# Kernel optimization log

Hardware: AMD Instinct MI355X
Metric: run time of the kernel (lower is better)

## Reference

```python
import jax, jax.numpy as jnp
import numpy as np

# Model config (matches init_kwargs)
DIM = 2048
INTER = 1408          # moe_inter_dim
E = 16                # n_routed_experts
TOPK = 4              # n_activated_experts
G = 4                 # n_expert_groups
TOPK_G = 2            # n_limited_groups
N_SHARED = 2
SHARED_INTER = N_SHARED * INTER  # 2816
ROUTE_SCALE = 1.0


def setup_inputs() -> dict:
    key = jax.random.key(0)
    ks = jax.random.split(key, 8)
    s = 0.02
    x = jax.random.normal(ks[0], (1, 2048, DIM), dtype=jnp.float32)
    Wg = jax.random.normal(ks[1], (E, DIM), dtype=jnp.float32) * s      # gate weight
    W1 = jax.random.normal(ks[2], (E, INTER, DIM), dtype=jnp.float32) * s  # expert gate proj
    W3 = jax.random.normal(ks[3], (E, INTER, DIM), dtype=jnp.float32) * s  # expert up proj
    W2 = jax.random.normal(ks[4], (E, DIM, INTER), dtype=jnp.float32) * s  # expert down proj
    Ws1 = jax.random.normal(ks[5], (SHARED_INTER, DIM), dtype=jnp.float32) * s
    Ws3 = jax.random.normal(ks[6], (SHARED_INTER, DIM), dtype=jnp.float32) * s
    Ws2 = jax.random.normal(ks[7], (DIM, SHARED_INTER), dtype=jnp.float32) * s
    return {"x": x, "Wg": Wg, "W1": W1, "W3": W3, "W2": W2,
            "Ws1": Ws1, "Ws3": Ws3, "Ws2": Ws2}


def _moe_forward(x, Wg, W1, W3, W2, Ws1, Ws3, Ws2):
    B, S, D = x.shape
    xt = x.reshape(-1, D)              # [T, D]
    T = xt.shape[0]

    # ---- Gate: group-limited top-k routing (bias is None since dim != 7168) ----
    scores = jax.nn.softmax(xt @ Wg.T, axis=-1)          # [T, E]
    sg = scores.reshape(T, G, E // G)                    # [T, G, E/G]
    group_scores = sg.max(axis=-1)                       # amax per group
    gidx = jax.lax.top_k(group_scores, TOPK_G)[1]        # [T, TOPK_G]
    gmask = jax.nn.one_hot(gidx, G, dtype=jnp.float32).sum(axis=1) > 0  # [T, G] kept groups
    masked = jnp.where(gmask[:, :, None], sg, -jnp.inf).reshape(T, E)
    topi = jax.lax.top_k(masked, TOPK)[1]                # [T, TOPK] expert indices
    weights = jnp.take_along_axis(scores, topi, axis=1) * ROUTE_SCALE  # original_scores gather

    # ---- Routed experts: dense per-expert SwiGLU FFN, zero-weight combine ----
    # combine[t, e] = sum over k of weights[t, k] * (topi[t, k] == e)
    combine = jnp.zeros((T, E), xt.dtype).at[jnp.arange(T)[:, None], topi].add(weights)
    h = jax.nn.silu(jnp.einsum('td,eid->eti', xt, W1)) * jnp.einsum('td,eid->eti', xt, W3)
    expert_out = jnp.einsum('eti,edi->etd', h, W2)       # [E, T, D]
    y = jnp.einsum('etd,te->td', expert_out, combine)    # [T, D]

    # ---- Shared expert (applied to all tokens) ----
    z = (jax.nn.silu(xt @ Ws1.T) * (xt @ Ws3.T)) @ Ws2.T

    return (y + z).reshape(B, S, D)


def reference(x, Wg, W1, W3, W2, Ws1, Ws3, Ws2):
    return _moe_forward(x, Wg, W1, W3, W2, Ws1, Ws3, Ws2)
```

## Files before the change

kernel.cpp:

```cpp
#include <hip/hip_runtime.h>
#include <stdint.h>

#define D_MODEL  2048
#define N_INTER  1408
#define SH_INTER 2816
#define T_TOK    2048
#define NSLOT    (T_TOK * 4)
#define MIB(x)   ((size_t)(x) << 20)

typedef __attribute__((ext_vector_type(8))) short bf16x8;
typedef __attribute__((ext_vector_type(4))) float f32x4;

__device__ __forceinline__ unsigned short f2bf(float f){
  unsigned int b = __builtin_bit_cast(unsigned int, f);
  b = (b + 0x7FFFu + ((b >> 16) & 1u)) >> 16;
  return (unsigned short)b;
}
__device__ __forceinline__ float bf2f(unsigned short h){
  unsigned int b = ((unsigned int)h) << 16;
  return __builtin_bit_cast(float, b);
}

#define GLOAD16(gp, lp) __builtin_amdgcn_global_load_lds( \
    (const __attribute__((address_space(1))) unsigned int*)(gp), \
    (__attribute__((address_space(3))) unsigned int*)(lp), 16, 0, 0)

__global__ void cvt_bf16_kernel(const float* __restrict__ x,
                                unsigned short* __restrict__ o, int n4){
  const int stride = gridDim.x * blockDim.x;
  for (int i = blockIdx.x * blockDim.x + threadIdx.x; i < n4; i += stride){
    const float4 v = ((const float4*)x)[i];
    ushort4 u; u.x = f2bf(v.x); u.y = f2bf(v.y); u.z = f2bf(v.z); u.w = f2bf(v.w);
    ((ushort4*)o)[i] = u;
  }
}

__global__ void cvt4_kernel(const float* __restrict__ x,  const float* __restrict__ Ws1,
                            const float* __restrict__ Ws3, const float* __restrict__ Ws2,
                            unsigned short* __restrict__ xbf, unsigned short* __restrict__ S1,
                            unsigned short* __restrict__ S3,  unsigned short* __restrict__ S2){
  const int N0 = T_TOK * D_MODEL / 4;
  const int NW = SH_INTER * D_MODEL / 4;
  const int total = N0 + 3 * NW;
  const int stride = gridDim.x * blockDim.x;
  for (int i = blockIdx.x * blockDim.x + threadIdx.x; i < total; i += stride){
    const float4* s; ushort4* d; int j;
    if (i < N0)            { s = (const float4*)x;   d = (ushort4*)xbf; j = i; }
    else if (i < N0 + NW)  { s = (const float4*)Ws1; d = (ushort4*)S1;  j = i - N0; }
    else if (i < N0 + 2*NW){ s = (const float4*)Ws3; d = (ushort4*)S3;  j = i - N0 - NW; }
    else                   { s = (const float4*)Ws2; d = (ushort4*)S2;  j = i - N0 - 2*NW; }
    const float4 v = s[j];
    ushort4 u; u.x = f2bf(v.x); u.y = f2bf(v.y); u.z = f2bf(v.z); u.w = f2bf(v.w);
    d[j] = u;
  }
}

__global__ void gate_kernel(const float* __restrict__ x, const float* __restrict__ Wg,
                            int* __restrict__ cnt, int* __restrict__ list,
                            float* __restrict__ wslot){
  const int t = blockIdx.x;
  const int l = threadIdx.x;
  const int e = l & 15, q = l >> 4;
  const float* xr = x + (size_t)t * D_MODEL + q * 512;
  const float* wr = Wg + (size_t)e * D_MODEL + q * 512;
  float p = 0.f;
  #pragma unroll 4
  for (int i = 0; i < 512; i += 4){
    float4 xv = *(const float4*)(xr + i);
    float4 wv = *(const float4*)(wr + i);
    p += xv.x*wv.x + xv.y*wv.y + xv.z*wv.z + xv.w*wv.w;
  }
  p += __shfl_xor(p, 16);
  p += __shfl_xor(p, 32);
  float mx = p;
  for (int d = 1; d < 16; d <<= 1) mx = fmaxf(mx, __shfl_xor(mx, d));
  float ex = __expf(p - mx);
  float sum = ex;
  for (int d = 1; d < 16; d <<= 1) sum += __shfl_xor(sum, d);
  const float sc = ex / sum;
  float gm = fmaxf(sc, __shfl_xor(sc, 1));
  gm = fmaxf(gm, __shfl_xor(gm, 2));
  const float g0 = __shfl(gm, 0), g1 = __shfl(gm, 4),
              g2 = __shfl(gm, 8), g3 = __shfl(gm, 12);
  const int grp = e >> 2;
  const float gs[4] = {g0, g1, g2, g3};
  int grank = 0;
  #pragma unroll
  for (int j = 0; j < 4; ++j)
    if (gs[j] > gm || (gs[j] == gm && j < grp)) grank++;
  const float msc = (grank < 2) ? sc : -INFINITY;
  int erank = 0;
  #pragma unroll
  for (int j = 0; j < 16; ++j){
    const float oj = __shfl(msc, j);
    if (oj > msc || (oj == msc && j < e)) erank++;
  }
  if (q == 0 && erank < 4 && msc > -INFINITY){
    const int pos = atomicAdd(&cnt[e], 1);
    const int slot = (t << 2) | erank;
    list[e * T_TOK + pos] = slot;
    wslot[slot] = sc;
  }
}

template<int MODE, int KS>
__global__ __launch_bounds__(512, 2)
void gemm8_kernel(const unsigned short* __restrict__ A,
                  const unsigned short* __restrict__ BG,
                  const unsigned short* __restrict__ BU,
                  void* __restrict__ OutP,
                  const int* __restrict__ list,
                  const int* __restrict__ cnt,
                  int K, int N, int NI, int MT, int NT)
{
  constexpr bool GATHER = (MODE == 2 || MODE == 3);
  constexpr bool GU     = (MODE == 0 || MODE == 2);
  __shared__ unsigned short As[3 * 8192];
  __shared__ unsigned short Bs[3 * 8192];

  const int per = gridDim.x >> 3;
  const int gsw = (blockIdx.x & 7) * per + (blockIdx.x >> 3);
  const int mt = gsw % MT;
  const int rest = gsw / MT;
  const int nt = rest % NT;
  const int rest2 = rest / NT;
  const int ks = (KS > 1) ? (rest2 % KS) : 0;
  const int e  = GATHER ? rest2 : 0;
  const int cntE = GATHER ? cnt[e] : (MT * 256);
  if (mt * 256 >= cntE) return;

  const int tid = threadIdx.x, wid = tid >> 6, lane = tid & 63;
  const int sx   = ((lane & 3) ^ ((lane >> 3) & 3)) << 3;
  const int kOff = (KS > 1) ? ks * (K / KS) : 0;

  const int rt0 = 32 * wid + (lane >> 2), rt1 = rt0 + 16;
  int ar0, ar1;
  if (GATHER){
    const int lim = cntE - 1;
    int p0 = mt * 256 + rt0; p0 = p0 < lim ? p0 : lim;
    int p1 = mt * 256 + rt1; p1 = p1 < lim ? p1 : lim;
    const int e0 = list[e * T_TOK + p0], e1 = list[e * T_TOK + p1];
    ar0 = (MODE == 2) ? (e0 >> 2) : e0;
    ar1 = (MODE == 2) ? (e1 >> 2) : e1;
  } else { ar0 = mt * 256 + rt0; ar1 = mt * 256 + rt1; }
  const unsigned short* pa0 = A + (size_t)ar0 * K + kOff + sx;
  const unsigned short* pa1 = A + (size_t)ar1 * K + kOff + sx;

  const unsigned short* pb0;
  const unsigned short* pb1;
  if (GU){
    const size_t eo = GATHER ? (size_t)e * NI * K : 0;
    const int g0 = nt * 256 + rt0, g1 = nt * 256 + rt1;
    pb0 = (g0 < NI ? BG + eo + (size_t)g0 * K : BU + eo + (size_t)(g0 - NI) * K) + sx;
    pb1 = (g1 < NI ? BG + eo + (size_t)g1 * K : BU + eo + (size_t)(g1 - NI) * K) + sx;
  } else {
    const unsigned short* base = BG + (GATHER ? (size_t)e * N * K : 0) + kOff;
    pb0 = base + (size_t)(nt * 256 + rt0) * K + sx;
    pb1 = base + (size_t)(nt * 256 + rt1) * K + sx;
  }

  const int w0 = (32 * wid) * 32, w1 = w0 + 512;
  const int bufStr = 8192;

  const int wm = wid >> 2, wn = wid & 3, lr = lane & 15, lq = lane >> 4;
  const int fx = (lq ^ ((lr >> 1) & 3)) << 3;
  int aoff[8], boff[4];
  #pragma unroll
  for (int m = 0; m < 8; ++m) aoff[m] = (wm * 128 + m * 16 + lr) * 32 + fx;
  #pragma unroll
  for (int n = 0; n < 4; ++n) boff[n] = (wn * 64 + n * 16 + lr) * 32 + fx;

  f32x4 acc[8][4];
  const f32x4 zero = {0.f, 0.f, 0.f, 0.f};
  #pragma unroll
  for (int m = 0; m < 8; ++m)
    #pragma unroll
    for (int n = 0; n < 4; ++n) acc[m][n] = zero;

  const int KT = (K / (KS > 1 ? KS : 1)) >> 5;
  #pragma unroll
  for (int t = 0; t < 3; ++t){
    GLOAD16(pa0, As + t * bufStr + w0);
    GLOAD16(pa1, As + t * bufStr + w1);
    GLOAD16(pb0, Bs + t * bufStr + w0);
    GLOAD16(pb1, Bs + t * bufStr + w1);
    pa0 += 32; pa1 += 32; pb0 += 32; pb1 += 32;
  }
  int c = 0;

  for (int kt = 0; kt < KT; ++kt){
    if (kt < KT - 2)       asm volatile("s_waitcnt vmcnt(8)" ::: "memory");
    else if (kt == KT - 2) asm volatile("s_waitcnt vmcnt(4)" ::: "memory");
    else                   asm volatile("s_waitcnt vmcnt(0)" ::: "memory");
    __builtin_amdgcn_s_barrier();

    const unsigned short* aC = As + c * bufStr;
    const unsigned short* bC = Bs + c * bufStr;
    bf16x8 af[8], bf[4];
    #pragma unroll
    for (int m = 0; m < 8; ++m) af[m] = *(const bf16x8*)(aC + aoff[m]);
    #pragma unroll
    for (int n = 0; n < 4; ++n) bf[n] = *(const bf16x8*)(bC + boff[n]);

    asm volatile("s_waitcnt lgkmcnt(0)" ::: "memory");
    __builtin_amdgcn_sched_barrier(0);
    __builtin_amdgcn_s_barrier();

    if (kt + 3 < KT){
      GLOAD16(pa0, As + c * bufStr + w0);
      GLOAD16(pa1, As + c * bufStr + w1);
      GLOAD16(pb0, Bs + c * bufStr + w0);
      GLOAD16(pb1, Bs + c * bufStr + w1);
      pa0 += 32; pa1 += 32; pb0 += 32; pb1 += 32;
    }

    __builtin_amdgcn_s_setprio(1);
    #pragma unroll
    for (int n = 0; n < 4; ++n)
      #pragma unroll
      for (int m = 0; m < 8; ++m)
        acc[m][n] = __builtin_amdgcn_mfma_f32_16x16x32_bf16(af[m], bf[n], acc[m][n], 0, 0, 0);
    __builtin_amdgcn_s_setprio(0);

    c = (c == 2) ? 0 : c + 1;
  }

  const int colBase = nt * 256 + wn * 64;
  #pragma unroll
  for (int m = 0; m < 8; ++m){
    #pragma unroll
    for (int r = 0; r < 4; ++r){
      const int grow = mt * 256 + wm * 128 + m * 16 + lq * 4 + r;
      if (MODE == 1){
        float* op = (float*)OutP + (size_t)ks * MT * 256 * N + (size_t)grow * N + colBase;
        #pragma unroll
        for (int n = 0; n < 4; ++n) op[n * 16 + lr] = acc[m][n][r];
      } else if (MODE == 0){
        unsigned short* op = (unsigned short*)OutP + (size_t)grow * N + colBase;
        #pragma unroll
        for (int n = 0; n < 4; ++n) op[n * 16 + lr] = f2bf(acc[m][n][r]);
      } else {
        if (grow >= cntE) continue;
        const int orow = list[e * T_TOK + grow];
        unsigned short* op = (unsigned short*)OutP + (size_t)orow * N + colBase;
        #pragma unroll
        for (int n = 0; n < 4; ++n) op[n * 16 + lr] = f2bf(acc[m][n][r]);
      }
    }
  }
}

__global__ void swiglu_split_kernel(const unsigned short* __restrict__ GU,
                                    unsigned short* __restrict__ H,
                                    int n8, int NI8){
  const int stride = gridDim.x * blockDim.x;
  for (int i = blockIdx.x * blockDim.x + threadIdx.x; i < n8; i += stride){
    const int r = i / NI8, ccol = i - r * NI8;
    const bf16x8 g = ((const bf16x8*)GU)[(size_t)r * 2 * NI8 + ccol];
    const bf16x8 u = ((const bf16x8*)GU)[(size_t)r * 2 * NI8 + NI8 + ccol];
    bf16x8 h;
    #pragma unroll
    for (int j = 0; j < 8; ++j){
      const float gv = bf2f((unsigned short)g[j]);
      const float uv = bf2f((unsigned short)u[j]);
      h[j] = (short)f2bf(gv / (1.f + __expf(-gv)) * uv);
    }
    ((bf16x8*)H)[i] = h;
  }
}

__global__ void combine_kernel(const unsigned short* __restrict__ H2,
                               const float* __restrict__ P,
                               const float* __restrict__ wslot,
                               float* __restrict__ out){
  const int t = blockIdx.x;
  const int ccol = threadIdx.x * 8;
  float w[4];
  #pragma unroll
  for (int k = 0; k < 4; ++k) w[k] = wslot[t * 4 + k];
  float a[8];
  #pragma unroll
  for (int j = 0; j < 8; ++j) a[j] = 0.f;
  #pragma unroll
  for (int p = 0; p < 4; ++p){
    const float* pp = P + (size_t)(p * T_TOK + t) * D_MODEL + ccol;
    #pragma unroll
    for (int j = 0; j < 8; ++j) a[j] += pp[j];
  }
  #pragma unroll
  for (int k = 0; k < 4; ++k){
    const bf16x8 hv = *(const bf16x8*)(H2 + (size_t)(t * 4 + k) * D_MODEL + ccol);
    #pragma unroll
    for (int j = 0; j < 8; ++j) a[j] += w[k] * bf2f((unsigned short)hv[j]);
  }
  float* o = out + (size_t)t * D_MODEL + ccol;
  #pragma unroll
  for (int j = 0; j < 8; ++j) o[j] = a[j];
}

extern "C" void kernel_launch(void* const* d_in, const int* in_sizes, int n_in,
                              void* d_out, int out_size, void* d_ws, size_t ws_size,
                              hipStream_t stream)
{
  const float* x   = (const float*)d_in[0];
  const float* Wg  = (const float*)d_in[1];
  const float* W1  = (const float*)d_in[2];
  const float* W3  = (const float*)d_in[3];
  const float* W2  = (const float*)d_in[4];
  const float* Ws1 = (const float*)d_in[5];
  const float* Ws3 = (const float*)d_in[6];
  const float* Ws2 = (const float*)d_in[7];
  float* out = (float*)d_out;

  char* ws = (char*)d_ws;
  int*   cnt   = (int*)(ws);
  int*   list  = (int*)(ws + 4096);
  float* wslot = (float*)(ws + 4096 + 131072);
  unsigned short* xbf  = (unsigned short*)(ws + MIB(1));
  unsigned short* S1   = (unsigned short*)(ws + MIB(10));
  unsigned short* S3   = (unsigned short*)(ws + MIB(22));
  unsigned short* S2   = (unsigned short*)(ws + MIB(34));
  unsigned short* Hs   = (unsigned short*)(ws + MIB(46));
  unsigned short* GU_s = (unsigned short*)(ws + MIB(58));
  unsigned short* Hr   = (unsigned short*)(ws + MIB(82));
  unsigned short* Hc   = (unsigned short*)(ws + MIB(129));
  unsigned short* H2   = (unsigned short*)(ws + MIB(153));
  float*          P    = (float*)        (ws + MIB(187));
  unsigned short* W1b  = (unsigned short*)(ws + MIB(255));
  unsigned short* W3b  = (unsigned short*)(ws + MIB(348));
  unsigned short* W2b  = (unsigned short*)(ws + MIB(441));

  const int NW_R = 16 * N_INTER * D_MODEL / 4;

  hipMemsetAsync(cnt, 0, 4096, stream);
  cvt4_kernel<<<2048, 256, 0, stream>>>(x, Ws1, Ws3, Ws2, xbf, S1, S3, S2);
  gate_kernel<<<T_TOK, 64, 0, stream>>>(x, Wg, cnt, list, wslot);

  gemm8_kernel<0, 1><<<176, 512, 0, stream>>>(xbf, S1, S3, GU_s, nullptr, nullptr,
                                              D_MODEL, 2 * SH_INTER, SH_INTER, 8, 22);
  cvt_bf16_kernel<<<4096, 256, 0, stream>>>(W1, W1b, NW_R);
  cvt_bf16_kernel<<<4096, 256, 0, stream>>>(W3, W3b, NW_R);
  swiglu_split_kernel<<<2048, 256, 0, stream>>>(GU_s, Hs, T_TOK * SH_INTER / 8, SH_INTER / 8);

  gemm8_kernel<1, 4><<<256, 512, 0, stream>>>(Hs, S2, nullptr, P, nullptr, nullptr,
                                              SH_INTER, D_MODEL, 0, 8, 8);

  gemm8_kernel<2, 1><<<1408, 512, 0, stream>>>(xbf, W1b, W3b, Hr, list, cnt,
                                               D_MODEL, 2 * N_INTER, N_INTER, 8, 11);
  cvt_bf16_kernel<<<4096, 256, 0, stream>>>(W2, W2b, NW_R);
  swiglu_split_kernel<<<2048, 256, 0, stream>>>(Hr, Hc, NSLOT * N_INTER / 8, N_INTER / 8);

  gemm8_kernel<3, 1><<<1024, 512, 0, stream>>>(Hc, W2b, nullptr, H2, list, cnt,
                                               N_INTER, D_MODEL, 0, 8, 8);

  combine_kernel<<<T_TOK, 256, 0, stream>>>(H2, P, wslot, out);
}
```

Baseline: 734.6 us.

## Restructure GEMM into double-buffered 64-wide K pipeline with concatenated gate/up weights

Measured after the change: 624.7 us. 15.0% less time.

```diff
diff --git a/kernel.cpp b/kernel.cpp
--- a/kernel.cpp
+++ b/kernel.cpp
@@ -32,6 +32,19 @@
     const float4 v = ((const float4*)x)[i];
     ushort4 u; u.x = f2bf(v.x); u.y = f2bf(v.y); u.z = f2bf(v.z); u.w = f2bf(v.w);
     ((ushort4*)o)[i] = u;
+  }
+}
+
+__global__ void cvt_routed_kernel(const float* __restrict__ src,
+                                  unsigned short* __restrict__ dst,
+                                  int n4, int nik4, int off4){
+  const int stride = gridDim.x * blockDim.x;
+  for (int i = blockIdx.x * blockDim.x + threadIdx.x; i < n4; i += stride){
+    const int e = i / nik4;
+    const int r = i - e * nik4;
+    const float4 v = ((const float4*)src)[i];
+    ushort4 u; u.x = f2bf(v.x); u.y = f2bf(v.y); u.z = f2bf(v.z); u.w = f2bf(v.w);
+    ((ushort4*)dst)[(size_t)e * 2 * nik4 + off4 + r] = u;
   }
 }
 
@@ -104,160 +117,189 @@
 }
 
 template<int MODE, int KS>
-__global__ __launch_bounds__(512, 2)
-void gemm8_kernel(const unsigned short* __restrict__ A,
-                  const unsigned short* __restrict__ BG,
-                  const unsigned short* __restrict__ BU,
-                  void* __restrict__ OutP,
-                  const int* __restrict__ list,
-                  const int* __restrict__ cnt,
-                  int K, int N, int NI, int MT, int NT)
+__global__ __launch_bounds__(512, 1)
+void gemm8p_kernel(const unsigned short* __restrict__ A,
+                   const unsigned short* __restrict__ B,
+                   void* __restrict__ OutP,
+                   const int* __restrict__ list,
+                   const int* __restrict__ cnt,
+                   int K, int N, int Astride, size_t eBstride,
+                   int MT, int NT)
 {
   constexpr bool GATHER = (MODE == 2 || MODE == 3);
-  constexpr bool GU     = (MODE == 0 || MODE == 2);
-  __shared__ unsigned short As[3 * 8192];
-  __shared__ unsigned short Bs[3 * 8192];
+  __shared__ unsigned short LDS[65536];
 
   const int per = gridDim.x >> 3;
   const int gsw = (blockIdx.x & 7) * per + (blockIdx.x >> 3);
   const int mt = gsw % MT;
-  const int rest = gsw / MT;
-  const int nt = rest % NT;
-  const int rest2 = rest / NT;
-  const int ks = (KS > 1) ? (rest2 % KS) : 0;
-  const int e  = GATHER ? rest2 : 0;
+  int rest = gsw / MT;
+  const int nt = rest % NT; rest /= NT;
+  const int ks = (KS > 1) ? (rest % KS) : 0;
+  const int e  = GATHER ? ((KS > 1) ? rest / KS : rest) : 0;
   const int cntE = GATHER ? cnt[e] : (MT * 256);
   if (mt * 256 >= cntE) return;
 
   const int tid = threadIdx.x, wid = tid >> 6, lane = tid & 63;
-  const int sx   = ((lane & 3) ^ ((lane >> 3) & 3)) << 3;
   const int kOff = (KS > 1) ? ks * (K / KS) : 0;
-
-  const int rt0 = 32 * wid + (lane >> 2), rt1 = rt0 + 16;
-  int ar0, ar1;
-  if (GATHER){
-    const int lim = cntE - 1;
-    int p0 = mt * 256 + rt0; p0 = p0 < lim ? p0 : lim;
-    int p1 = mt * 256 + rt1; p1 = p1 < lim ? p1 : lim;
-    const int e0 = list[e * T_TOK + p0], e1 = list[e * T_TOK + p1];
-    ar0 = (MODE == 2) ? (e0 >> 2) : e0;
-    ar1 = (MODE == 2) ? (e1 >> 2) : e1;
-  } else { ar0 = mt * 256 + rt0; ar1 = mt * 256 + rt1; }
-  const unsigned short* pa0 = A + (size_t)ar0 * K + kOff + sx;
-  const unsigned short* pa1 = A + (size_t)ar1 * K + kOff + sx;
-
-  const unsigned short* pb0;
-  const unsigned short* pb1;
-  if (GU){
-    const size_t eo = GATHER ? (size_t)e * NI * K : 0;
-    const int g0 = nt * 256 + rt0, g1 = nt * 256 + rt1;
-    pb0 = (g0 < NI ? BG + eo + (size_t)g0 * K : BU + eo + (size_t)(g0 - NI) * K) + sx;
-    pb1 = (g1 < NI ? BG + eo + (size_t)g1 * K : BU + eo + (size_t)(g1 - NI) * K) + sx;
-  } else {
-    const unsigned short* base = BG + (GATHER ? (size_t)e * N * K : 0) + kOff;
-    pb0 = base + (size_t)(nt * 256 + rt0) * K + sx;
-    pb1 = base + (size_t)(nt * 256 + rt1) * K + sx;
-  }
-
-  const int w0 = (32 * wid) * 32, w1 = w0 + 512;
-  const int bufStr = 8192;
+  const int sx = ((lane & 3) ^ ((lane >> 3) & 3)) << 3;
+
+  const unsigned short* pa[2];
+  const unsigned short* pb[2];
+  const unsigned short* Bb = B + (GATHER ? (size_t)e * eBstride : 0);
+  #pragma unroll
+  for (int j = 0; j < 2; ++j){
+    const int rl = (2 * wid + j) * 16 + (lane >> 2);
+    int ga;
+    if (GATHER){
+      int p = mt * 256 + rl;
+      const int lim = cntE - 1;
+      p = p < lim ? p : lim;
+      const int en = list[e * T_TOK + p];
+      ga = (MODE == 2) ? (en >> 2) : en;
+    } else ga = mt * 256 + rl;
+    pa[j] = A + (size_t)ga * Astride + kOff + sx;
+    pb[j] = Bb + (size_t)(nt * 256 + rl) * K + kOff + sx;
+  }
+  const int dW0 = (2 * wid) * 512, dW1 = dW0 + 512;
 
   const int wm = wid >> 2, wn = wid & 3, lr = lane & 15, lq = lane >> 4;
   const int fx = (lq ^ ((lr >> 1) & 3)) << 3;
-  int aoff[8], boff[4];
-  #pragma unroll
-  for (int m = 0; m < 8; ++m) aoff[m] = (wm * 128 + m * 16 + lr) * 32 + fx;
-  #pragma unroll
-  for (int n = 0; n < 4; ++n) boff[n] = (wn * 64 + n * 16 + lr) * 32 + fx;
+  int aoff0[4], aoff1[4], boff[4];
+  #pragma unroll
+  for (int m = 0; m < 4; ++m){
+    aoff0[m] = (wm * 128 + m * 16 + lr) * 32 + fx;
+    aoff1[m] = (wm * 128 + 64 + m * 16 + lr) * 32 + fx;
+  }
+  #pragma unroll
+  for (int n = 0; n < 4; ++n) boff[n] = 16384 + (wn * 64 + n * 16 + lr) * 32 + fx;
 
   f32x4 acc[8][4];
   const f32x4 zero = {0.f, 0.f, 0.f, 0.f};
   #pragma unroll
-  for (int m = 0; m < 8; ++m)
-    #pragma unroll
-    for (int n = 0; n < 4; ++n) acc[m][n] = zero;
-
-  const int KT = (K / (KS > 1 ? KS : 1)) >> 5;
-  #pragma unroll
-  for (int t = 0; t < 3; ++t){
-    GLOAD16(pa0, As + t * bufStr + w0);
-    GLOAD16(pa1, As + t * bufStr + w1);
-    GLOAD16(pb0, Bs + t * bufStr + w0);
-    GLOAD16(pb1, Bs + t * bufStr + w1);
-    pa0 += 32; pa1 += 32; pb0 += 32; pb1 += 32;
-  }
-  int c = 0;
-
-  for (int kt = 0; kt < KT; ++kt){
-    if (kt < KT - 2)       asm volatile("s_waitcnt vmcnt(8)" ::: "memory");
-    else if (kt == KT - 2) asm volatile("s_waitcnt vmcnt(4)" ::: "memory");
-    else                   asm volatile("s_waitcnt vmcnt(0)" ::: "memory");
-    __builtin_amdgcn_s_barrier();
-
-    const unsigned short* aC = As + c * bufStr;
-    const unsigned short* bC = Bs + c * bufStr;
-    bf16x8 af[8], bf[4];
-    #pragma unroll
-    for (int m = 0; m < 8; ++m) af[m] = *(const bf16x8*)(aC + aoff[m]);
-    #pragma unroll
-    for (int n = 0; n < 4; ++n) bf[n] = *(const bf16x8*)(bC + boff[n]);
-
+  for (int M = 0; M < 8; ++M)
+    #pragma unroll
+    for (int n = 0; n < 4; ++n) acc[M][n] = zero;
+
+  const int KT = (K / (KS > 1 ? KS : 1)) >> 6;
+
+  GLOAD16(pa[0],      &LDS[dW0]);
+  GLOAD16(pa[1],      &LDS[dW1]);
+  GLOAD16(pb[0],      &LDS[16384 + dW0]);
+  GLOAD16(pb[1],      &LDS[16384 + dW1]);
+  GLOAD16(pa[0] + 32, &LDS[8192 + dW0]);
+  GLOAD16(pa[1] + 32, &LDS[8192 + dW1]);
+  GLOAD16(pb[0] + 32, &LDS[16384 + 8192 + dW0]);
+  GLOAD16(pb[1] + 32, &LDS[16384 + 8192 + dW1]);
+
+  for (int t = 0; t < KT; ++t){
+    const int bb = (t & 1) << 15;
+    const int db = bb ^ 32768;
+    const bool more = (t + 1) < KT;
+    const size_t ko = (size_t)(t + 1) * 64;
+    bf16x8 af[4], bq[4];
+
+    asm volatile("s_waitcnt vmcnt(4)" ::: "memory");
+    __builtin_amdgcn_s_barrier();
+    #pragma unroll
+    for (int m = 0; m < 4; ++m) af[m] = *(const bf16x8*)(&LDS[bb + aoff0[m]]);
+    #pragma unroll
+    for (int n = 0; n < 4; ++n) bq[n] = *(const bf16x8*)(&LDS[bb + boff[n]]);
+    if (more){ GLOAD16(pa[0] + ko, &LDS[db + dW0]); GLOAD16(pa[1] + ko, &LDS[db + dW1]); }
     asm volatile("s_waitcnt lgkmcnt(0)" ::: "memory");
     __builtin_amdgcn_sched_barrier(0);
-    __builtin_amdgcn_s_barrier();
-
-    if (kt + 3 < KT){
-      GLOAD16(pa0, As + c * bufStr + w0);
-      GLOAD16(pa1, As + c * bufStr + w1);
-      GLOAD16(pb0, Bs + c * bufStr + w0);
-      GLOAD16(pb1, Bs + c * bufStr + w1);
-      pa0 += 32; pa1 += 32; pb0 += 32; pb1 += 32;
-    }
-
     __builtin_amdgcn_s_setprio(1);
     #pragma unroll
     for (int n = 0; n < 4; ++n)
       #pragma unroll
-      for (int m = 0; m < 8; ++m)
-        acc[m][n] = __builtin_amdgcn_mfma_f32_16x16x32_bf16(af[m], bf[n], acc[m][n], 0, 0, 0);
+      for (int m = 0; m < 4; ++m)
+        acc[m][n] = __builtin_amdgcn_mfma_f32_16x16x32_bf16(af[m], bq[n], acc[m][n], 0, 0, 0);
     __builtin_amdgcn_s_setprio(0);
-
-    c = (c == 2) ? 0 : c + 1;
+    __builtin_amdgcn_s_barrier();
+
+    #pragma unroll
+    for (int m = 0; m < 4; ++m) af[m] = *(const bf16x8*)(&LDS[bb + aoff1[m]]);
+    if (more){ GLOAD16(pb[0] + ko, &LDS[db + 16384 + dW0]);
+               GLOAD16(pb[1] + ko, &LDS[db + 16384 + dW1]); }
+    asm volatile("s_waitcnt lgkmcnt(0)" ::: "memory");
+    __builtin_amdgcn_sched_barrier(0);
+    __builtin_amdgcn_s_setprio(1);
+    #pragma unroll
+    for (int n = 0; n < 4; ++n)
+      #pragma unroll
+      for (int m = 0; m < 4; ++m)
+        acc[4 + m][n] = __builtin_amdgcn_mfma_f32_16x16x32_bf16(af[m], bq[n], acc[4 + m][n], 0, 0, 0);
+    __builtin_amdgcn_s_setprio(0);
+    __builtin_amdgcn_s_barrier();
+
+    if (more) asm volatile("s_waitcnt vmcnt(4)" ::: "memory");
+    else      asm volatile("s_waitcnt vmcnt(0)" ::: "memory");
+    __builtin_amdgcn_s_barrier();
+    #pragma unroll
+    for (int m = 0; m < 4; ++m) af[m] = *(const bf16x8*)(&LDS[bb + 8192 + aoff0[m]]);
+    #pragma unroll
+    for (int n = 0; n < 4; ++n) bq[n] = *(const bf16x8*)(&LDS[bb + 8192 + boff[n]]);
+    if (more){ GLOAD16(pa[0] + ko + 32, &LDS[db + 8192 + dW0]);
+               GLOAD16(pa[1] + ko + 32, &LDS[db + 8192 + dW1]); }
+    asm volatile("s_waitcnt lgkmcnt(0)" ::: "memory");
+    __builtin_amdgcn_sched_barrier(0);
+    __builtin_amdgcn_s_setprio(1);
+    #pragma unroll
+    for (int n = 0; n < 4; ++n)
+      #pragma unroll
+      for (int m = 0; m < 4; ++m)
+        acc[m][n] = __builtin_amdgcn_mfma_f32_16x16x32_bf16(af[m], bq[n], acc[m][n], 0, 0, 0);
+    __builtin_amdgcn_s_setprio(0);
+    __builtin_amdgcn_s_barrier();
+
+    #pragma unroll
+    for (int m = 0; m < 4; ++m) af[m] = *(const bf16x8*)(&LDS[bb + 8192 + aoff1[m]]);
+    if (more){ GLOAD16(pb[0] + ko + 32, &LDS[db + 16384 + 8192 + dW0]);
+               GLOAD16(pb[1] + ko + 32, &LDS[db + 16384 + 8192 + dW1]); }
+    asm volatile("s_waitcnt lgkmcnt(0)" ::: "memory");
+    __builtin_amdgcn_sched_barrier(0);
+    __builtin_amdgcn_s_setprio(1);
+    #pragma unroll
+    for (int n = 0; n < 4; ++n)
+      #pragma unroll
+      for (int m = 0; m < 4; ++m)
+        acc[4 + m][n] = __builtin_amdgcn_mfma_f32_16x16x32_bf16(af[m], bq[n], acc[4 + m][n], 0, 0, 0);
+    __builtin_amdgcn_s_setprio(0);
+    __builtin_amdgcn_s_barrier();
   }
 
   const int colBase = nt * 256 + wn * 64;
   #pragma unroll
-  for (int m = 0; m < 8; ++m){
+  for (int M = 0; M < 8; ++M){
     #pragma unroll
     for (int r = 0; r < 4; ++r){
-      const int grow = mt * 256 + wm * 128 + m * 16 + lq * 4 + r;
+      const int grow = mt * 256 + wm * 128 + (M >> 2) * 64 + (M & 3) * 16 + lq * 4 + r;
       if (MODE == 1){
         float* op = (float*)OutP + (size_t)ks * MT * 256 * N + (size_t)grow * N + colBase;
         #pragma unroll
-        for (int n = 0; n < 4; ++n) op[n * 16 + lr] = acc[m][n][r];
+        for (int n = 0; n < 4; ++n) op[n * 16 + lr] = acc[M][n][r];
       } else if (MODE == 0){
         unsigned short* op = (unsigned short*)OutP + (size_t)grow * N + colBase;
         #pragma unroll
-        for (int n = 0; n < 4; ++n) op[n * 16 + lr] = f2bf(acc[m][n][r]);
+        for (int n = 0; n < 4; ++n) op[n * 16 + lr] = f2bf(acc[M][n][r]);
       } else {
         if (grow >= cntE) continue;
         const int orow = list[e * T_TOK + grow];
         unsigned short* op = (unsigned short*)OutP + (size_t)orow * N + colBase;
         #pragma unroll
-        for (int n = 0; n < 4; ++n) op[n * 16 + lr] = f2bf(acc[m][n][r]);
+        for (int n = 0; n < 4; ++n) op[n * 16 + lr] = f2bf(acc[M][n][r]);
       }
     }
   }
 }
 
-__global__ void swiglu_split_kernel(const unsigned short* __restrict__ GU,
-                                    unsigned short* __restrict__ H,
-                                    int n8, int NI8){
+__global__ void swiglu_ip_kernel(unsigned short* __restrict__ GU, int n8, int NI8){
   const int stride = gridDim.x * blockDim.x;
+  bf16x8* p = (bf16x8*)GU;
   for (int i = blockIdx.x * blockDim.x + threadIdx.x; i < n8; i += stride){
     const int r = i / NI8, ccol = i - r * NI8;
-    const bf16x8 g = ((const bf16x8*)GU)[(size_t)r * 2 * NI8 + ccol];
-    const bf16x8 u = ((const bf16x8*)GU)[(size_t)r * 2 * NI8 + NI8 + ccol];
+    const size_t gi = (size_t)r * 2 * NI8 + ccol;
+    const bf16x8 g = p[gi];
+    const bf16x8 u = p[gi + NI8];
     bf16x8 h;
     #pragma unroll
     for (int j = 0; j < 8; ++j){
@@ -265,7 +307,7 @@
       const float uv = bf2f((unsigned short)u[j]);
       h[j] = (short)f2bf(gv / (1.f + __expf(-gv)) * uv);
     }
-    ((bf16x8*)H)[i] = h;
+    p[gi] = h;
   }
 }
 
@@ -318,40 +360,43 @@
   float* wslot = (float*)(ws + 4096 + 131072);
   unsigned short* xbf  = (unsigned short*)(ws + MIB(1));
   unsigned short* S1   = (unsigned short*)(ws + MIB(10));
-  unsigned short* S3   = (unsigned short*)(ws + MIB(22));
+  unsigned short* S3   = S1 + (size_t)SH_INTER * D_MODEL;
   unsigned short* S2   = (unsigned short*)(ws + MIB(34));
-  unsigned short* Hs   = (unsigned short*)(ws + MIB(46));
-  unsigned short* GU_s = (unsigned short*)(ws + MIB(58));
-  unsigned short* Hr   = (unsigned short*)(ws + MIB(82));
-  unsigned short* Hc   = (unsigned short*)(ws + MIB(129));
-  unsigned short* H2   = (unsigned short*)(ws + MIB(153));
-  float*          P    = (float*)        (ws + MIB(187));
-  unsigned short* W1b  = (unsigned short*)(ws + MIB(255));
-  unsigned short* W3b  = (unsigned short*)(ws + MIB(348));
-  unsigned short* W2b  = (unsigned short*)(ws + MIB(441));
-
-  const int NW_R = 16 * N_INTER * D_MODEL / 4;
+  unsigned short* GU_s = (unsigned short*)(ws + MIB(46));
+  unsigned short* Hr   = (unsigned short*)(ws + MIB(70));
+  unsigned short* H2   = (unsigned short*)(ws + MIB(118));
+  float*          P    = (float*)        (ws + MIB(152));
+  unsigned short* WGU  = (unsigned short*)(ws + MIB(220));
+  unsigned short* W2b  = (unsigned short*)(ws + MIB(405));
+  const int NW_R  = 16 * N_INTER * D_MODEL / 4;
+  const int NIK4  = N_INTER * D_MODEL / 4;
 
   hipMemsetAsync(cnt, 0, 4096, stream);
   cvt4_kernel<<<2048, 256, 0, stream>>>(x, Ws1, Ws3, Ws2, xbf, S1, S3, S2);
   gate_kernel<<<T_TOK, 64, 0, stream>>>(x, Wg, cnt, list, wslot);
 
-  gemm8_kernel<0, 1><<<176, 512, 0, stream>>>(xbf, S1, S3, GU_s, nullptr, nullptr,
-                                              D_MODEL, 2 * SH_INTER, SH_INTER, 8, 22);
-  cvt_bf16_kernel<<<4096, 256, 0, stream>>>(W1, W1b, NW_R);
-  cvt_bf16_kernel<<<4096, 256, 0, stream>>>(W3, W3b, NW_R);
-  swiglu_split_kernel<<<2048, 256, 0, stream>>>(GU_s, Hs, T_TOK * SH_INTER / 8, SH_INTER / 8);
-
-  gemm8_kernel<1, 4><<<256, 512, 0, stream>>>(Hs, S2, nullptr, P, nullptr, nullptr,
-                                              SH_INTER, D_MODEL, 0, 8, 8);
-
-  gemm8_kernel<2, 1><<<1408, 512, 0, stream>>>(xbf, W1b, W3b, Hr, list, cnt,
-                                               D_MODEL, 2 * N_INTER, N_INTER, 8, 11);
+  gemm8p_kernel<0, 1><<<176, 512, 0, stream>>>(
+      xbf, S1, GU_s, nullptr, nullptr,
+      D_MODEL, 2 * SH_INTER, D_MODEL, 0, 8, 22);
+  swiglu_ip_kernel<<<2048, 256, 0, stream>>>(GU_s, T_TOK * SH_INTER / 8, SH_INTER / 8);
+
+  gemm8p_kernel<1, 4><<<256, 512, 0, stream>>>(
+      GU_s, S2, P, nullptr, nullptr,
+      SH_INTER, D_MODEL, 2 * SH_INTER, 0, 8, 8);
+
+  cvt_routed_kernel<<<4096, 256, 0, stream>>>(W1, WGU, NW_R, NIK4, 0);
+  cvt_routed_kernel<<<4096, 256, 0, stream>>>(W3, WGU, NW_R, NIK4, NIK4);
+
+  gemm8p_kernel<2, 1><<<1408, 512, 0, stream>>>(
+      xbf, WGU, Hr, list, cnt,
+      D_MODEL, 2 * N_INTER, D_MODEL, (size_t)2 * N_INTER * D_MODEL, 8, 11);
+  swiglu_ip_kernel<<<2048, 256, 0, stream>>>(Hr, NSLOT * N_INTER / 8, N_INTER / 8);
+
   cvt_bf16_kernel<<<4096, 256, 0, stream>>>(W2, W2b, NW_R);
-  swiglu_split_kernel<<<2048, 256, 0, stream>>>(Hr, Hc, NSLOT * N_INTER / 8, N_INTER / 8);
-
-  gemm8_kernel<3, 1><<<1024, 512, 0, stream>>>(Hc, W2b, nullptr, H2, list, cnt,
-                                               N_INTER, D_MODEL, 0, 8, 8);
+
+  gemm8p_kernel<3, 1><<<1024, 512, 0, stream>>>(
+      Hr, W2b, H2, list, cnt,
+      N_INTER, D_MODEL, 2 * N_INTER, (size_t)D_MODEL * N_INTER, 8, 8);
 
   combine_kernel<<<T_TOK, 256, 0, stream>>>(H2, P, wslot, out);
 }
```
